# Kernel optimization log

Hardware: AMD Instinct MI355X
Metric: run time of the kernel (lower is better)

The kernel has to match this reference:

```python
import jax, jax.numpy as jnp
import numpy as np

BS, NS, NSTEP = 128, 1024, 8
IN_DIM, HID, MLP = 768, 512, 512
NEG = -100000.0


def setup_inputs() -> dict:
    key = jax.random.key(0)
    ks = jax.random.split(key, 12)
    s_h = 1.0 / np.sqrt(HID)
    s_cat = 1.0 / np.sqrt(HID + IN_DIM)
    s_m = 1.0 / np.sqrt(MLP)
    # gumbel noise implements Categorical sampling as argmax(logits + gumbel)
    u = jax.random.uniform(ks[9], (NSTEP, BS, NS), jnp.float32, 1e-7, 1.0 - 1e-7)
    return {
        "target_emb": jax.random.normal(ks[0], (BS, IN_DIM), jnp.float32),
        "ctx_emb": jax.random.normal(ks[1], (BS, NS, IN_DIM), jnp.float32),
        "target_len": jax.random.randint(ks[2], (BS,), 1, 32),
        "ctx_len": jax.random.randint(ks[3], (BS,), NSTEP, NS + 1),
        "n_step": NSTEP,
        "W_ih": jax.random.normal(ks[4], (4 * HID, IN_DIM), jnp.float32) * s_h,
        "W_hh": jax.random.normal(ks[5], (4 * HID, HID), jnp.float32) * s_h,
        "b_ih": jnp.zeros((4 * HID,), jnp.float32),
        "b_hh": jnp.zeros((4 * HID,), jnp.float32),
        "W1c": jax.random.normal(ks[6], (MLP, IN_DIM), jnp.float32) * s_cat,
        "W1h": jax.random.normal(ks[7], (MLP, HID), jnp.float32) * s_cat,
        "b1": jnp.zeros((MLP,), jnp.float32),
        "w2": jax.random.normal(ks[8], (MLP,), jnp.float32) * s_m,
        "b2": jnp.zeros((), jnp.float32),
        "gumbel": -jnp.log(-jnp.log(u)),
    }


def reference(target_emb, ctx_emb, target_len, ctx_len, n_step,
              W_ih, W_hh, b_ih, b_hh, W1c, W1h, b1, w2, b2, gumbel):
    bs, ns, in_dim = ctx_emb.shape
    hid = W_hh.shape[1]
    # mlp1 split: ctx part is constant across steps (concat([ctx, h]) @ W1^T = ctx@W1c^T + h@W1h^T)
    ctx_part = jnp.einsum('bnd,md->bnm', ctx_emb, W1c) + b1  # [bs, ns, mlp]
    mask0 = jnp.where(jnp.arange(ns)[None, :] >= ctx_len[:, None], NEG, 0.0).astype(jnp.float32)
    h0 = jnp.zeros((bs, hid), jnp.float32)
    c0 = jnp.zeros((bs, hid), jnp.float32)
    lp0 = jnp.zeros((bs,), jnp.float32)
    batch_idx = jnp.arange(bs)

    def step(carry, g):
        h, c, mask, x, lp = carry
        # LSTMCell (torch gate order: i, f, g, o); dropout is identity (eval semantics)
        gates = x @ W_ih.T + b_ih + h @ W_hh.T + b_hh
        i_g, f_g, g_g, o_g = jnp.split(gates, 4, axis=-1)
        c_new = jax.nn.sigmoid(f_g) * c + jax.nn.sigmoid(i_g) * jnp.tanh(g_g)
        h_new = jax.nn.sigmoid(o_g) * jnp.tanh(c_new)
        # attention-style MLP score
        pre = ctx_part + (h_new @ W1h.T)[:, None, :]          # [bs, ns, mlp]
        sc = jnp.tanh(pre) @ w2 + b2 + mask                   # [bs, ns]
        # Categorical(probs=softmax(sc)).sample() via Gumbel-argmax
        out = jnp.argmax(sc + g, axis=-1)                     # [bs]
        lp = lp + jnp.take_along_axis(jax.nn.log_softmax(sc, axis=-1), out[:, None], 1)[:, 0]
        mask = mask.at[batch_idx, out].set(NEG)
        x_new = jnp.take_along_axis(ctx_emb, out[:, None, None], axis=1)[:, 0, :]
        return (h_new, c_new, mask, x_new, lp), out

    (h, c, mask, x, log_probs), outputs = jax.lax.scan(
        step, (h0, c0, mask0, target_emb, lp0), gumbel)
    return outputs, log_probs
```

## Files before the change

kernel.cpp:

```cpp
#include <hip/hip_runtime.h>
#include <hip/hip_bf16.h>

#define BSZ 128
#define NSQ 1024
#define NSTEPC 8
#define IND 768
#define HIDD 512
#define G4D 2048
#define MLPD 512
#define KXD 1280
#define NEGV -100000.0f
#define KSG 16
#define KSH 8
#define MSPLIT 4

typedef __attribute__((ext_vector_type(4))) float f32x4;
typedef __attribute__((ext_vector_type(8))) short short8v;

__device__ __forceinline__ void gl16(const unsigned short* g, unsigned short* l) {
  __builtin_amdgcn_global_load_lds(
      (const __attribute__((address_space(1))) unsigned int*)(g),
      (__attribute__((address_space(3))) unsigned int*)(l), 16, 0, 0);
}

__device__ __forceinline__ void split2(float4 f0, float4 f1, short8v& hi, short8v& lo) {
  float fv[8] = {f0.x, f0.y, f0.z, f0.w, f1.x, f1.y, f1.z, f1.w};
#pragma unroll
  for (int j = 0; j < 8; ++j) {
    const unsigned ub = __builtin_bit_cast(unsigned, fv[j]);
    const unsigned hb = ub & 0xFFFF0000u;
    const float lf = fv[j] - __builtin_bit_cast(float, hb);
    hi[j] = (short)(hb >> 16);
    lo[j] = (short)(__builtin_bit_cast(unsigned, lf) >> 16);
  }
}

__device__ __forceinline__ float tanh_fast(float x) {
  x = fminf(fmaxf(x, -15.0f), 15.0f);
  float e = __builtin_amdgcn_exp2f(x * 2.8853900817779268f);
  float r = __builtin_amdgcn_rcpf(e + 1.0f);
  return fmaf(-2.0f, r, 1.0f);
}

__global__ __launch_bounds__(256) void k_prep_w1c(
    const float* __restrict__ W1c,
    unsigned short* __restrict__ wch, unsigned short* __restrict__ wcl) {
  const int c = blockIdx.x * 256 + threadIdx.x;
  if (c >= 49152) return;
  const int row = c / 96, wc = c - row * 96;
  const int tile = wc >> 2, c4 = wc & 3;
  const int slot = c4 ^ ((row >> 1) & 3);
  const size_t unit = ((size_t)((row >> 7) * 24 + tile) * 128 + (row & 127)) * 4 + slot;
  const float* src = W1c + (size_t)row * IND + wc * 8;
  const float4 f0 = *(const float4*)src, f1 = *(const float4*)(src + 4);
  short8v hi, lo;
  split2(f0, f1, hi, lo);
  *(short8v*)(wch + unit * 8) = hi;
  *(short8v*)(wcl + unit * 8) = lo;
}

__global__ __launch_bounds__(256) void k_init(
    const float* __restrict__ te, const int* __restrict__ cl,
    float* __restrict__ mask, float* __restrict__ xh,
    float* __restrict__ cst, float* __restrict__ lp) {
  const int b = blockIdx.x, tid = threadIdx.x;
  const int L = cl[b];
  for (int n = tid; n < NSQ; n += 256) mask[(size_t)b*NSQ + n] = (n >= L) ? NEGV : 0.0f;
  for (int d = tid; d < IND; d += 256) xh[(size_t)b*KXD + d] = te[(size_t)b*IND + d];
  for (int j = tid; j < HIDD; j += 256) {
    xh[(size_t)b*KXD + IND + j] = 0.0f;
    cst[(size_t)b*HIDD + j] = 0.0f;
  }
  if (tid == 0) lp[b] = 0.0f;
}

__global__ __launch_bounds__(256) void k_ctx5(
    const float* __restrict__ ctx,
    const unsigned short* __restrict__ wch, const unsigned short* __restrict__ wcl,
    const float* __restrict__ bias, const int* __restrict__ clen,
    float* __restrict__ cp) {
  __shared__ __align__(16) unsigned short sWh[2][4096], sWl[2][4096];
  __shared__ __align__(16) unsigned short sCh[2][4096], sCl[2][4096];
  const int bid = blockIdx.x;
  const int v = ((bid & 7) << 9) + (bid >> 3);
  const int mx = v & 3;
  const int rbC = v >> 2;
  const int b = rbC >> 3;
  const int nbase = (rbC & 7) << 7;
  if (nbase >= clen[b]) return;
  const int i0 = rbC << 7;
  const int m0 = mx << 7;
  const int tid = threadIdx.x;
  const int lane = tid & 63, wid = tid >> 6;
  const int wm = wid & 1, wn = wid >> 1;
  const int l15 = lane & 15, l4 = lane >> 4;
  const int c0r = tid >> 2, cs = tid & 3;
  const int c1r = 64 + c0r;
  const int k0rd = cs ^ ((c0r >> 1) & 3);
  const int k1rd = cs ^ ((c1r >> 1) & 3);
  const float* csrc0 = ctx + (size_t)(i0 + c0r) * IND + k0rd * 8;
  const float* csrc1 = ctx + (size_t)(i0 + c1r) * IND + k1rd * 8;

#pragma unroll
  for (int i = 0; i < 4; ++i) {
    const int seg = wid * 4 + i;
    const unsigned short* g = ((seg & 8) ? wcl : wch) +
        (size_t)(mx * 24) * 4096 + (seg & 7) * 512 + lane * 8;
    unsigned short* l = ((seg & 8) ? sWl[0] : sWh[0]) + (seg & 7) * 512;
    gl16(g, l);
  }
  {
    short8v hi, lo;
    split2(*(const float4*)csrc0, *(const float4*)(csrc0 + 4), hi, lo);
    *(short8v*)&sCh[0][tid * 8] = hi;
    *(short8v*)&sCl[0][tid * 8] = lo;
    split2(*(const float4*)csrc1, *(const float4*)(csrc1 + 4), hi, lo);
    *(short8v*)&sCh[0][(256 + tid) * 8] = hi;
    *(short8v*)&sCl[0][(256 + tid) * 8] = lo;
  }
  __syncthreads();

  f32x4 acc[4][4] = {};
  for (int t = 0; t < 24; ++t) {
    const int cur = t & 1, nb = cur ^ 1;
    float4 r00, r01, r10, r11;
    if (t + 1 < 24) {
#pragma unroll
      for (int i = 0; i < 4; ++i) {
        const int seg = wid * 4 + i;
        const unsigned short* g = ((seg & 8) ? wcl : wch) +
            (size_t)(mx * 24 + t + 1) * 4096 + (seg & 7) * 512 + lane * 8;
        unsigned short* l = ((seg & 8) ? sWl[nb] : sWh[nb]) + (seg & 7) * 512;
        gl16(g, l);
      }
      r00 = *(const float4*)(csrc0 + (t + 1) * 32);
      r01 = *(const float4*)(csrc0 + (t + 1) * 32 + 4);
      r10 = *(const float4*)(csrc1 + (t + 1) * 32);
      r11 = *(const float4*)(csrc1 + (t + 1) * 32 + 4);
    }
    short8v ah[4], al[4], bh[4], bl[4];
#pragma unroll
    for (int f = 0; f < 4; ++f) {
      const int rw = wm * 64 + f * 16 + l15;
      const int so = (l4 ^ ((rw >> 1) & 3)) << 3;
      ah[f] = *(const short8v*)&sWh[cur][rw * 32 + so];
      al[f] = *(const short8v*)&sWl[cur][rw * 32 + so];
      const int rc = wn * 64 + f * 16 + l15;
      const int sc = (l4 ^ ((rc >> 1) & 3)) << 3;
      bh[f] = *(const short8v*)&sCh[cur][rc * 32 + sc];
      bl[f] = *(const short8v*)&sCl[cur][rc * 32 + sc];
    }
#pragma unroll
    for (int fm = 0; fm < 4; ++fm)
#pragma unroll
      for (int fn = 0; fn < 4; ++fn) {
        acc[fm][fn] = __builtin_amdgcn_mfma_f32_16x16x32_bf16(ah[fm], bh[fn], acc[fm][fn], 0, 0, 0);
        acc[fm][fn] = __builtin_amdgcn_mfma_f32_16x16x32_bf16(ah[fm], bl[fn], acc[fm][fn], 0, 0, 0);
        acc[fm][fn] = __builtin_amdgcn_mfma_f32_16x16x32_bf16(al[fm], bh[fn], acc[fm][fn], 0, 0, 0);
      }
    if (t + 1 < 24) {
      short8v hi, lo;
      split2(r00, r01, hi, lo);
      *(short8v*)&sCh[nb][tid * 8] = hi;
      *(short8v*)&sCl[nb][tid * 8] = lo;
      split2(r10, r11, hi, lo);
      *(short8v*)&sCh[nb][(256 + tid) * 8] = hi;
      *(short8v*)&sCl[nb][(256 + tid) * 8] = lo;
    }
    __syncthreads();
  }
#pragma unroll
  for (int fm = 0; fm < 4; ++fm) {
#pragma unroll
    for (int r = 0; r < 4; ++r) {
      const int m = m0 + wm * 64 + fm * 16 + l4 * 4 + r;
      const float bb = bias[m];
      float* dst = cp + (((size_t)(b * MLPD + m)) << 10) + nbase + wn * 64 + l15;
#pragma unroll
      for (int fn = 0; fn < 4; ++fn)
        dst[fn * 16] = acc[fm][fn][r] + bb;
    }
  }
}

__global__ __launch_bounds__(256) void k_pgemm(
    const float* __restrict__ A, int lda, int acol,
    const float* __restrict__ B0, int ldb0, int kb,
    const float* __restrict__ B1, int ldb1,
    int kTiles, int N, float* __restrict__ P) {
  __shared__ float As[16][128];
  __shared__ float Bs[16][132];
  const int n0 = blockIdx.x * 128;
  const int kc0 = blockIdx.y * kTiles * 16;
  const int tid = threadIdx.x;
  const int tn = tid & 15;
  const int ta = tid >> 4;
  float acc[8][8] = {};
  for (int t = 0; t < kTiles; ++t) {
    const int k0 = kc0 + t * 16;
#pragma unroll
    for (int u = 0; u < 2; ++u) {
      const int v = tid + u * 256;
      const int r = v >> 2, kc = v & 3;
      const float4 a4 = *(const float4*)(A + (size_t)r * lda + acol + k0 + kc * 4);
      As[kc*4+0][r] = a4.x; As[kc*4+1][r] = a4.y; As[kc*4+2][r] = a4.z; As[kc*4+3][r] = a4.w;
      const float* bp = (k0 < kb) ? (B0 + (size_t)(n0 + r) * ldb0 + k0 + kc * 4)
                                  : (B1 + (size_t)(n0 + r) * ldb1 + (k0 - kb) + kc * 4);
      const float4 b4 = *(const float4*)bp;
      Bs[kc*4+0][r] = b4.x; Bs[kc*4+1][r] = b4.y; Bs[kc*4+2][r] = b4.z; Bs[kc*4+3][r] = b4.w;
    }
    __syncthreads();
#pragma unroll
    for (int kk = 0; kk < 16; ++kk) {
      float av[8], bv[8];
#pragma unroll
      for (int q = 0; q < 8; ++q) av[q] = As[kk][ta*8+q];
#pragma unroll
      for (int q = 0; q < 8; ++q) bv[q] = Bs[kk][tn*8+q];
#pragma unroll
      for (int ri = 0; ri < 8; ++ri)
#pragma unroll
        for (int ni = 0; ni < 8; ++ni)
          acc[ri][ni] = fmaf(av[ri], bv[ni], acc[ri][ni]);
    }
    __syncthreads();
  }
#pragma unroll
  for (int ri = 0; ri < 8; ++ri) {
    const int i = ta * 8 + ri;
    float* p = P + ((size_t)blockIdx.y * BSZ + i) * N + n0 + tn * 8;
    *(float4*)(p + 0) = make_float4(acc[ri][0], acc[ri][1], acc[ri][2], acc[ri][3]);
    *(float4*)(p + 4) = make_float4(acc[ri][4], acc[ri][5], acc[ri][6], acc[ri][7]);
  }
}

__global__ __launch_bounds__(512) void k_lstm(
    const float* __restrict__ gp, const float* __restrict__ b_ih,
    const float* __restrict__ b_hh, float* __restrict__ cst, float* __restrict__ xh) {
  const int b = blockIdx.x, j = threadIdx.x;
  float g[4];
#pragma unroll
  for (int q = 0; q < 4; ++q) {
    float s = b_ih[q*HIDD + j] + b_hh[q*HIDD + j];
#pragma unroll
    for (int ks = 0; ks < KSG; ++ks) s += gp[((size_t)ks*BSZ + b)*G4D + q*HIDD + j];
    g[q] = s;
  }
  const float c_old = cst[(size_t)b*HIDD + j];
  const float ig = 1.0f / (1.0f + expf(-g[0]));
  const float fg = 1.0f / (1.0f + expf(-g[1]));
  const float gg = tanhf(g[2]);
  const float og = 1.0f / (1.0f + expf(-g[3]));
  const float cn = fg * c_old + ig * gg;
  const float hn = og * tanhf(cn);
  cst[(size_t)b*HIDD + j] = cn;
  xh[(size_t)b*KXD + IND + j] = hn;
}

__global__ __launch_bounds__(256) void k_scores(
    const float* __restrict__ cp, const float* __restrict__ hpp,
    const float* __restrict__ w2, const int* __restrict__ clen,
    float* __restrict__ psc) {
  const int mh = blockIdx.x;
  const int b = blockIdx.y;
  const int tid = threadIdx.x;
  __shared__ float hs[128], ws[128];
  if (tid < 128) {
    const int m = mh * 128 + tid;
    float s = 0.0f;
#pragma unroll
    for (int ks = 0; ks < KSH; ++ks) s += hpp[((size_t)ks*BSZ + b)*MLPD + m];
    hs[tid] = s;
    ws[tid] = w2[m];
  }
  __syncthreads();
  const int len = clen[b];
  const int n0 = tid * 4;
  if (n0 >= len) return;
  float ax = 0, ay = 0, az = 0, aw = 0;
  const float* base = cp + ((size_t)b * MLPD + mh * 128) * NSQ + n0;
#pragma unroll 4
  for (int mm = 0; mm < 128; ++mm) {
    const float4 c4 = *(const float4*)(base + (size_t)mm * NSQ);
    const float h = hs[mm], w = ws[mm];
    ax = fmaf(tanh_fast(c4.x + h), w, ax);
    ay = fmaf(tanh_fast(c4.y + h), w, ay);
    az = fmaf(tanh_fast(c4.z + h), w, az);
    aw = fmaf(tanh_fast(c4.w + h), w, aw);
  }
  *(float4*)(psc + ((size_t)b * MSPLIT + mh) * NSQ + n0) = make_float4(ax, ay, az, aw);
}

__global__ __launch_bounds__(256) void k_argmax(
    const float* __restrict__ psc, float* __restrict__ mask,
    const float* __restrict__ gum, const float* __restrict__ b2p,
    float* __restrict__ lp, const float* __restrict__ ctx,
    float* __restrict__ xh, float* __restrict__ outv, int step) {
  const int b = blockIdx.x, tid = threadIdx.x;
  __shared__ float rv[256], rs[256], rm[256];
  __shared__ int ri[256];
  __shared__ int sel;
  const float b2 = b2p[0];
  const int n0 = tid * 4;
  const float4 m4 = *(const float4*)(mask + (size_t)b * NSQ + n0);
  float sc[4] = {b2 + m4.x, b2 + m4.y, b2 + m4.z, b2 + m4.w};
#pragma unroll
  for (int mh = 0; mh < MSPLIT; ++mh) {
    const float4 p4 = *(const float4*)(psc + ((size_t)b * MSPLIT + mh) * NSQ + n0);
    sc[0] += p4.x; sc[1] += p4.y; sc[2] += p4.z; sc[3] += p4.w;
  }
  const float4 g4 = *(const float4*)(gum + ((size_t)step * BSZ + b) * NSQ + n0);
  const float gv[4] = {g4.x, g4.y, g4.z, g4.w};
  float bestv = -1e30f, bests = 0.0f, msc = -1e30f;
  int bestn = 0;
#pragma unroll
  for (int q = 0; q < 4; ++q) {
    const float v = sc[q] + gv[q];
    if (v > bestv) { bestv = v; bestn = n0 + q; bests = sc[q]; }
    msc = fmaxf(msc, sc[q]);
  }
  rv[tid] = bestv; ri[tid] = bestn; rs[tid] = bests; rm[tid] = msc;
  __syncthreads();
  for (int o = 128; o > 0; o >>= 1) {
    if (tid < o) {
      if (rv[tid+o] > rv[tid] || (rv[tid+o] == rv[tid] && ri[tid+o] < ri[tid])) {
        rv[tid] = rv[tid+o]; ri[tid] = ri[tid+o]; rs[tid] = rs[tid+o];
      }
      rm[tid] = fmaxf(rm[tid], rm[tid+o]);
    }
    __syncthreads();
  }
  const float M = rm[0];
  __syncthreads();
  float se = 0.0f;
#pragma unroll
  for (int q = 0; q < 4; ++q)
    se += __builtin_amdgcn_exp2f((sc[q] - M) * 1.4426950408889634f);
  rm[tid] = se;
  __syncthreads();
  for (int o = 128; o > 0; o >>= 1) {
    if (tid < o) rm[tid] += rm[tid+o];
    __syncthreads();
  }
  if (tid == 0) {
    const int n = ri[0];
    const float lse = M + logf(rm[0]);
    const float nlp = lp[b] + rs[0] - lse;
    lp[b] = nlp;
    mask[(size_t)b * NSQ + n] = NEGV;
    outv[step * BSZ + b] = (float)n;
    if (step == NSTEPC - 1) outv[NSTEPC * BSZ + b] = nlp;
    sel = n;
  }
  __syncthreads();
  const int n = sel;
  const float4* src = (const float4*)(ctx + ((size_t)b * NSQ + n) * IND);
  float4* dst = (float4*)(xh + (size_t)b * KXD);
  for (int d = tid; d < IND / 4; d += 256) dst[d] = src[d];
}

extern "C" void kernel_launch(void* const* d_in, const int* in_sizes, int n_in,
                              void* d_out, int out_size, void* d_ws, size_t ws_size,
                              hipStream_t stream) {
  const float* target_emb = (const float*)d_in[0];
  const float* ctx_emb   = (const float*)d_in[1];
  const int*   ctx_len   = (const int*)d_in[3];
  const float* W_ih = (const float*)d_in[5];
  const float* W_hh = (const float*)d_in[6];
  const float* b_ih = (const float*)d_in[7];
  const float* b_hh = (const float*)d_in[8];
  const float* W1c  = (const float*)d_in[9];
  const float* W1h  = (const float*)d_in[10];
  const float* b1   = (const float*)d_in[11];
  const float* w2   = (const float*)d_in[12];
  const float* b2   = (const float*)d_in[13];
  const float* gumbel = (const float*)d_in[14];
  float* out = (float*)d_out;

  float* ws = (float*)d_ws;
  size_t off = 0;
  auto alloc = [&](size_t n) { float* p = ws + off; off += (n + 63) & ~(size_t)63; return p; };

  float* cp   = alloc((size_t)BSZ * MLPD * NSQ);
  float* gp   = alloc((size_t)KSG * BSZ * G4D);
  float* hpp  = alloc((size_t)KSH * BSZ * MLPD);
  float* psc  = alloc((size_t)BSZ * MSPLIT * NSQ);
  float* mask = alloc((size_t)BSZ * NSQ);
  float* xh   = alloc((size_t)BSZ * KXD);
  float* cst  = alloc((size_t)BSZ * HIDD);
  float* lp   = alloc(128);
  unsigned short* wch = (unsigned short*)alloc(196608);
  unsigned short* wcl = (unsigned short*)alloc(196608);

  k_prep_w1c<<<192, 256, 0, stream>>>(W1c, wch, wcl);
  k_init<<<BSZ, 256, 0, stream>>>(target_emb, ctx_len, mask, xh, cst, lp);
  k_ctx5<<<4096, 256, 0, stream>>>(ctx_emb, wch, wcl, b1, ctx_len, cp);

  for (int t = 0; t < NSTEPC; ++t) {
    k_pgemm<<<dim3(G4D/128, KSG), 256, 0, stream>>>(
        xh, KXD, 0, W_ih, IND, IND, W_hh, HIDD, 5, G4D, gp);
    k_lstm<<<BSZ, 512, 0, stream>>>(gp, b_ih, b_hh, cst, xh);
    k_pgemm<<<dim3(MLPD/128, KSH), 256, 0, stream>>>(
        xh, KXD, IND, W1h, HIDD, 1 << 30, nullptr, 0, 4, MLPD, hpp);
    k_scores<<<dim3(MSPLIT, BSZ), 256, 0, stream>>>(cp, hpp, w2, ctx_len, psc);
    k_argmax<<<BSZ, 256, 0, stream>>>(psc, mask, gumbel, b2, lp, ctx_emb, xh, out, t);
  }
}
```

Measured before the change: 857.7 us.

## Drop LDS staging in ctx GEMM and fuse h@W1h into LSTM kernel

The context GEMM kernel stops staging operands through shared memory. W1c is pre-arranged into MFMA fragment order so each wave loads its A fragments straight from global memory, and the ctx rows are split into bf16 hi/lo in registers. This removes the LDS writes, double buffering and per-tile barriers, but gives up LDS-based reuse and relies on cache hits for reuse across waves. Separately, the per-step h@W1h^T product is folded into the LSTM kernel as a per-thread dot product over shared h, which removes one split-K GEMM launch and its partial-sum reduction per step. The cost is a 512-long serial dot per thread, with each thread reading its own W1h row.

```diff
diff --git a/kernel.cpp b/kernel.cpp
--- a/kernel.cpp
+++ b/kernel.cpp
@@ -11,17 +11,10 @@
 #define KXD 1280
 #define NEGV -100000.0f
 #define KSG 16
-#define KSH 8
 #define MSPLIT 4
 
 typedef __attribute__((ext_vector_type(4))) float f32x4;
 typedef __attribute__((ext_vector_type(8))) short short8v;
-
-__device__ __forceinline__ void gl16(const unsigned short* g, unsigned short* l) {
-  __builtin_amdgcn_global_load_lds(
-      (const __attribute__((address_space(1))) unsigned int*)(g),
-      (__attribute__((address_space(3))) unsigned int*)(l), 16, 0, 0);
-}
 
 __device__ __forceinline__ void split2(float4 f0, float4 f1, short8v& hi, short8v& lo) {
   float fv[8] = {f0.x, f0.y, f0.z, f0.w, f1.x, f1.y, f1.z, f1.w};
@@ -42,21 +35,22 @@
   return fmaf(-2.0f, r, 1.0f);
 }
 
-__global__ __launch_bounds__(256) void k_prep_w1c(
+__global__ __launch_bounds__(256) void k_prep_wfrag(
     const float* __restrict__ W1c,
-    unsigned short* __restrict__ wch, unsigned short* __restrict__ wcl) {
+    unsigned short* __restrict__ wfh, unsigned short* __restrict__ wfl) {
   const int c = blockIdx.x * 256 + threadIdx.x;
   if (c >= 49152) return;
   const int row = c / 96, wc = c - row * 96;
-  const int tile = wc >> 2, c4 = wc & 3;
-  const int slot = c4 ^ ((row >> 1) & 3);
-  const size_t unit = ((size_t)((row >> 7) * 24 + tile) * 128 + (row & 127)) * 4 + slot;
+  const int mxwm = row >> 6;
+  const int f = (row >> 4) & 3, l15 = row & 15;
+  const int t = wc >> 2, l4 = wc & 3;
+  const size_t unit = (((size_t)(mxwm * 24 + t) * 4 + f) * 64) + l4 * 16 + l15;
   const float* src = W1c + (size_t)row * IND + wc * 8;
   const float4 f0 = *(const float4*)src, f1 = *(const float4*)(src + 4);
   short8v hi, lo;
   split2(f0, f1, hi, lo);
-  *(short8v*)(wch + unit * 8) = hi;
-  *(short8v*)(wcl + unit * 8) = lo;
+  *(short8v*)(wfh + unit * 8) = hi;
+  *(short8v*)(wfl + unit * 8) = lo;
 }
 
 __global__ __launch_bounds__(256) void k_init(
@@ -74,13 +68,11 @@
   if (tid == 0) lp[b] = 0.0f;
 }
 
-__global__ __launch_bounds__(256) void k_ctx5(
+__global__ __launch_bounds__(256) void k_ctx6(
     const float* __restrict__ ctx,
-    const unsigned short* __restrict__ wch, const unsigned short* __restrict__ wcl,
+    const unsigned short* __restrict__ wfh, const unsigned short* __restrict__ wfl,
     const float* __restrict__ bias, const int* __restrict__ clen,
     float* __restrict__ cp) {
-  __shared__ __align__(16) unsigned short sWh[2][4096], sWl[2][4096];
-  __shared__ __align__(16) unsigned short sCh[2][4096], sCl[2][4096];
   const int bid = blockIdx.x;
   const int v = ((bid & 7) << 9) + (bid >> 3);
   const int mx = v & 3;
@@ -94,61 +86,24 @@
   const int lane = tid & 63, wid = tid >> 6;
   const int wm = wid & 1, wn = wid >> 1;
   const int l15 = lane & 15, l4 = lane >> 4;
-  const int c0r = tid >> 2, cs = tid & 3;
-  const int c1r = 64 + c0r;
-  const int k0rd = cs ^ ((c0r >> 1) & 3);
-  const int k1rd = cs ^ ((c1r >> 1) & 3);
-  const float* csrc0 = ctx + (size_t)(i0 + c0r) * IND + k0rd * 8;
-  const float* csrc1 = ctx + (size_t)(i0 + c1r) * IND + k1rd * 8;
-
-#pragma unroll
-  for (int i = 0; i < 4; ++i) {
-    const int seg = wid * 4 + i;
-    const unsigned short* g = ((seg & 8) ? wcl : wch) +
-        (size_t)(mx * 24) * 4096 + (seg & 7) * 512 + lane * 8;
-    unsigned short* l = ((seg & 8) ? sWl[0] : sWh[0]) + (seg & 7) * 512;
-    gl16(g, l);
-  }
-  {
-    short8v hi, lo;
-    split2(*(const float4*)csrc0, *(const float4*)(csrc0 + 4), hi, lo);
-    *(short8v*)&sCh[0][tid * 8] = hi;
-    *(short8v*)&sCl[0][tid * 8] = lo;
-    split2(*(const float4*)csrc1, *(const float4*)(csrc1 + 4), hi, lo);
-    *(short8v*)&sCh[0][(256 + tid) * 8] = hi;
-    *(short8v*)&sCl[0][(256 + tid) * 8] = lo;
-  }
-  __syncthreads();
+
+  const size_t wbase = (size_t)((mx * 2 + wm) * 24) * 2048 + lane * 8;
+  const float* cbase = ctx + (size_t)(i0 + wn * 64 + l15) * IND + l4 * 8;
 
   f32x4 acc[4][4] = {};
   for (int t = 0; t < 24; ++t) {
-    const int cur = t & 1, nb = cur ^ 1;
-    float4 r00, r01, r10, r11;
-    if (t + 1 < 24) {
-#pragma unroll
-      for (int i = 0; i < 4; ++i) {
-        const int seg = wid * 4 + i;
-        const unsigned short* g = ((seg & 8) ? wcl : wch) +
-            (size_t)(mx * 24 + t + 1) * 4096 + (seg & 7) * 512 + lane * 8;
-        unsigned short* l = ((seg & 8) ? sWl[nb] : sWh[nb]) + (seg & 7) * 512;
-        gl16(g, l);
-      }
-      r00 = *(const float4*)(csrc0 + (t + 1) * 32);
-      r01 = *(const float4*)(csrc0 + (t + 1) * 32 + 4);
-      r10 = *(const float4*)(csrc1 + (t + 1) * 32);
-      r11 = *(const float4*)(csrc1 + (t + 1) * 32 + 4);
-    }
-    short8v ah[4], al[4], bh[4], bl[4];
+    short8v bh[4], bl[4];
 #pragma unroll
     for (int f = 0; f < 4; ++f) {
-      const int rw = wm * 64 + f * 16 + l15;
-      const int so = (l4 ^ ((rw >> 1) & 3)) << 3;
-      ah[f] = *(const short8v*)&sWh[cur][rw * 32 + so];
-      al[f] = *(const short8v*)&sWl[cur][rw * 32 + so];
-      const int rc = wn * 64 + f * 16 + l15;
-      const int sc = (l4 ^ ((rc >> 1) & 3)) << 3;
-      bh[f] = *(const short8v*)&sCh[cur][rc * 32 + sc];
-      bl[f] = *(const short8v*)&sCl[cur][rc * 32 + sc];
+      const float* s = cbase + (size_t)(f * 16) * IND + t * 32;
+      split2(*(const float4*)s, *(const float4*)(s + 4), bh[f], bl[f]);
+    }
+    short8v ah[4], al[4];
+    const size_t toff = wbase + (size_t)t * 2048;
+#pragma unroll
+    for (int f = 0; f < 4; ++f) {
+      ah[f] = *(const short8v*)(wfh + toff + f * 512);
+      al[f] = *(const short8v*)(wfl + toff + f * 512);
     }
 #pragma unroll
     for (int fm = 0; fm < 4; ++fm)
@@ -158,16 +113,6 @@
         acc[fm][fn] = __builtin_amdgcn_mfma_f32_16x16x32_bf16(ah[fm], bl[fn], acc[fm][fn], 0, 0, 0);
         acc[fm][fn] = __builtin_amdgcn_mfma_f32_16x16x32_bf16(al[fm], bh[fn], acc[fm][fn], 0, 0, 0);
       }
-    if (t + 1 < 24) {
-      short8v hi, lo;
-      split2(r00, r01, hi, lo);
-      *(short8v*)&sCh[nb][tid * 8] = hi;
-      *(short8v*)&sCl[nb][tid * 8] = lo;
-      split2(r10, r11, hi, lo);
-      *(short8v*)&sCh[nb][(256 + tid) * 8] = hi;
-      *(short8v*)&sCl[nb][(256 + tid) * 8] = lo;
-    }
-    __syncthreads();
   }
 #pragma unroll
   for (int fm = 0; fm < 4; ++fm) {
@@ -234,9 +179,11 @@
   }
 }
 
-__global__ __launch_bounds__(512) void k_lstm(
+__global__ __launch_bounds__(512) void k_lstm2f(
     const float* __restrict__ gp, const float* __restrict__ b_ih,
-    const float* __restrict__ b_hh, float* __restrict__ cst, float* __restrict__ xh) {
+    const float* __restrict__ b_hh, const float* __restrict__ W1h,
+    float* __restrict__ cst, float* __restrict__ xh, float* __restrict__ hpp) {
+  __shared__ float hs[HIDD];
   const int b = blockIdx.x, j = threadIdx.x;
   float g[4];
 #pragma unroll
@@ -255,6 +202,17 @@
   const float hn = og * tanhf(cn);
   cst[(size_t)b*HIDD + j] = cn;
   xh[(size_t)b*KXD + IND + j] = hn;
+  hs[j] = hn;
+  __syncthreads();
+  const float* wr = W1h + (size_t)j * HIDD;
+  float s = 0.0f;
+#pragma unroll 4
+  for (int k = 0; k < HIDD; k += 4) {
+    const float4 h4 = *(const float4*)&hs[k];
+    const float4 w4 = *(const float4*)&wr[k];
+    s = fmaf(h4.x, w4.x, fmaf(h4.y, w4.y, fmaf(h4.z, w4.z, fmaf(h4.w, w4.w, s))));
+  }
+  hpp[(size_t)b * HIDD + j] = s;
 }
 
 __global__ __launch_bounds__(256) void k_scores(
@@ -266,12 +224,8 @@
   const int tid = threadIdx.x;
   __shared__ float hs[128], ws[128];
   if (tid < 128) {
-    const int m = mh * 128 + tid;
-    float s = 0.0f;
-#pragma unroll
-    for (int ks = 0; ks < KSH; ++ks) s += hpp[((size_t)ks*BSZ + b)*MLPD + m];
-    hs[tid] = s;
-    ws[tid] = w2[m];
+    hs[tid] = hpp[(size_t)b * MLPD + mh * 128 + tid];
+    ws[tid] = w2[mh * 128 + tid];
   }
   __syncthreads();
   const int len = clen[b];
@@ -383,25 +337,23 @@
 
   float* cp   = alloc((size_t)BSZ * MLPD * NSQ);
   float* gp   = alloc((size_t)KSG * BSZ * G4D);
-  float* hpp  = alloc((size_t)KSH * BSZ * MLPD);
+  float* hpp  = alloc((size_t)BSZ * MLPD);
   float* psc  = alloc((size_t)BSZ * MSPLIT * NSQ);
   float* mask = alloc((size_t)BSZ * NSQ);
   float* xh   = alloc((size_t)BSZ * KXD);
   float* cst  = alloc((size_t)BSZ * HIDD);
   float* lp   = alloc(128);
-  unsigned short* wch = (unsigned short*)alloc(196608);
-  unsigned short* wcl = (unsigned short*)alloc(196608);
-
-  k_prep_w1c<<<192, 256, 0, stream>>>(W1c, wch, wcl);
+  unsigned short* wfh = (unsigned short*)alloc(196608);
+  unsigned short* wfl = (unsigned short*)alloc(196608);
+
+  k_prep_wfrag<<<192, 256, 0, stream>>>(W1c, wfh, wfl);
   k_init<<<BSZ, 256, 0, stream>>>(target_emb, ctx_len, mask, xh, cst, lp);
-  k_ctx5<<<4096, 256, 0, stream>>>(ctx_emb, wch, wcl, b1, ctx_len, cp);
+  k_ctx6<<<4096, 256, 0, stream>>>(ctx_emb, wfh, wfl, b1, ctx_len, cp);
 
   for (int t = 0; t < NSTEPC; ++t) {
     k_pgemm<<<dim3(G4D/128, KSG), 256, 0, stream>>>(
         xh, KXD, 0, W_ih, IND, IND, W_hh, HIDD, 5, G4D, gp);
-    k_lstm<<<BSZ, 512, 0, stream>>>(gp, b_ih, b_hh, cst, xh);
-    k_pgemm<<<dim3(MLPD/128, KSH), 256, 0, stream>>>(
-        xh, KXD, IND, W1h, HIDD, 1 << 30, nullptr, 0, 4, MLPD, hpp);
+    k_lstm2f<<<BSZ, 512, 0, stream>>>(gp, b_ih, b_hh, W1h, cst, xh, hpp);
     k_scores<<<dim3(MSPLIT, BSZ), 256, 0, stream>>>(cp, hpp, w2, ctx_len, psc);
     k_argmax<<<BSZ, 256, 0, stream>>>(psc, mask, gumbel, b2, lp, ctx_emb, xh, out, t);
   }
```

Measured after the change: 994.5 us. 1.16x slower.
